# Kernel tuning notes

Hardware: AMD Instinct MI355X
Metric: run time of the kernel (lower is better)

## Reference

```python
import jax, jax.numpy as jnp
import numpy as np


def setup_inputs() -> dict:
    key = jax.random.key(0)
    ks = jax.random.split(key, 5)
    B, DEC, ENC, H = 4, 256, 1024, 256
    s = 1.0 / np.sqrt(H)
    return {
        "x_decoder": jax.random.normal(ks[0], (B, DEC, H), dtype=jnp.float32),
        "x_encoder": jax.random.normal(ks[1], (B, ENC, H), dtype=jnp.float32),
        "w1": jax.random.normal(ks[2], (H, H), dtype=jnp.float32) * s,
        "w2": jax.random.normal(ks[3], (H, H), dtype=jnp.float32) * s,
        "v": jax.random.normal(ks[4], (H,), dtype=jnp.float32) * s,
    }


def reference(x_decoder, x_encoder, w1, w2, v):
    # nn.Linear applies x @ W^T; weights here stored as (out, in) = (H, H)
    enc_t = jnp.einsum('beh,oh->beo', x_encoder, w1)   # (B, ENC, H)
    dec_t = jnp.einsum('bdh,oh->bdo', x_decoder, w2)   # (B, DEC, H)
    # Broadcast-add -> tanh -> dot with v: scores (B, DEC, ENC)
    scores = jnp.einsum('bdeh,h->bde',
                        jnp.tanh(dec_t[:, :, None, :] + enc_t[:, None, :, :]), v)
    return jax.nn.log_softmax(scores, axis=-1)
```

## Files before the change

kernel.cpp:

```cpp
#include <hip/hip_runtime.h>
#include <hip/hip_bf16.h>


#define B_ 4
#define DEC_ 256
#define ENC_ 1024
#define H_ 256

using bf16x8 = __attribute__((ext_vector_type(8))) short;
using f32x4 = __attribute__((ext_vector_type(4))) float;

__device__ inline short f2bf(float f) {
  union { float f; unsigned u; } x; x.f = f;
  return (short)((x.u + 0x8000u) >> 16);
}

#define LDK 72

__global__ __launch_bounds__(256) void gemm_mfma(
    const float* __restrict__ w1, const float* __restrict__ xe,
    const float* __restrict__ xd, const float* __restrict__ w2,
    float* __restrict__ encE, float* __restrict__ decE) {
  const int blk = blockIdx.x;
  const float* A;
  const float* Bsrc;
  float* C;
  int ldc, m0, n0;
  if (blk < 256) {
    const int b = blk >> 6;
    const int t = blk & 63;
    m0 = (t >> 4) << 6; n0 = (t & 15) << 6;
    A = w1;
    Bsrc = xe + (size_t)b * ENC_ * H_;
    C = encE + (size_t)b * H_ * ENC_;
    ldc = ENC_;
  } else {
    const int blk2 = blk - 256;
    const int b = blk2 >> 4;
    const int t = blk2 & 15;
    m0 = (t >> 2) << 6; n0 = (t & 3) << 6;
    A = xd + (size_t)b * DEC_ * H_;
    Bsrc = w2;
    C = decE + (size_t)b * DEC_ * H_;
    ldc = H_;
  }
  const int K = H_;
  const int tid = threadIdx.x;
  const int wave = tid >> 6, lane = tid & 63;
  const int wm = (wave >> 1) << 5, wn = (wave & 1) << 5;
  const int fr = lane & 15;
  const int fk = (lane >> 4) << 3;

  __shared__ short As[2][64][LDK];
  __shared__ short Bs[2][64][LDK];

  const int srow = tid >> 2;
  const int skq = (tid & 3) << 4;
  const float* ag = A + (size_t)(m0 + srow) * K + skq;
  const float* bg = Bsrc + (size_t)(n0 + srow) * K + skq;

  float4 ra[4], rb[4];
#define LDCHUNK(K0)                                                    \
  {                                                                    \
    _Pragma("unroll")                                                  \
    for (int i = 0; i < 4; ++i) {                                      \
      ra[i] = *(const float4*)(ag + (K0) + 4 * i);                     \
      rb[i] = *(const float4*)(bg + (K0) + 4 * i);                     \
    }                                                                  \
  }
#define STCHUNK(BUF)                                                   \
  {                                                                    \
    _Pragma("unroll")                                                  \
    for (int j = 0; j < 2; ++j) {                                      \
      bf16x8 pa, pb;                                                   \
      pa[0] = f2bf(ra[2 * j].x);     pa[1] = f2bf(ra[2 * j].y);        \
      pa[2] = f2bf(ra[2 * j].z);     pa[3] = f2bf(ra[2 * j].w);        \
      pa[4] = f2bf(ra[2 * j + 1].x); pa[5] = f2bf(ra[2 * j + 1].y);    \
      pa[6] = f2bf(ra[2 * j + 1].z); pa[7] = f2bf(ra[2 * j + 1].w);    \
      pb[0] = f2bf(rb[2 * j].x);     pb[1] = f2bf(rb[2 * j].y);        \
      pb[2] = f2bf(rb[2 * j].z);     pb[3] = f2bf(rb[2 * j].w);        \
      pb[4] = f2bf(rb[2 * j + 1].x); pb[5] = f2bf(rb[2 * j + 1].y);    \
      pb[6] = f2bf(rb[2 * j + 1].z); pb[7] = f2bf(rb[2 * j + 1].w);    \
      *(bf16x8*)&As[BUF][srow][skq + 8 * j] = pa;                      \
      *(bf16x8*)&Bs[BUF][srow][skq + 8 * j] = pb;                      \
    }                                                                  \
  }

  f32x4 acc[2][2] = {};

#define COMPUTE(BUF)                                                   \
  {                                                                    \
    _Pragma("unroll")                                                  \
    for (int kk = 0; kk < 2; ++kk) {                                   \
      bf16x8 af[2], bff[2];                                            \
      _Pragma("unroll")                                                \
      for (int mi = 0; mi < 2; ++mi)                                   \
        af[mi] = *(const bf16x8*)&As[BUF][wm + (mi << 4) + fr][(kk << 5) + fk]; \
      _Pragma("unroll")                                                \
      for (int ni = 0; ni < 2; ++ni)                                   \
        bff[ni] = *(const bf16x8*)&Bs[BUF][wn + (ni << 4) + fr][(kk << 5) + fk]; \
      _Pragma("unroll")                                                \
      for (int mi = 0; mi < 2; ++mi)                                   \
        _Pragma("unroll")                                              \
        for (int ni = 0; ni < 2; ++ni)                                 \
          acc[mi][ni] = __builtin_amdgcn_mfma_f32_16x16x32_bf16(       \
              af[mi], bff[ni], acc[mi][ni], 0, 0, 0);                  \
    }                                                                  \
  }

  LDCHUNK(0)
  STCHUNK(0)
  __syncthreads();
  LDCHUNK(64) COMPUTE(0) STCHUNK(1) __syncthreads();
  LDCHUNK(128) COMPUTE(1) STCHUNK(0) __syncthreads();
  LDCHUNK(192) COMPUTE(0) STCHUNK(1) __syncthreads();
  COMPUTE(1)

  const float SC = 2.8853900817779268f;
#pragma unroll
  for (int mi = 0; mi < 2; ++mi) {
#pragma unroll
    for (int ni = 0; ni < 2; ++ni) {
      const int row = m0 + wm + (mi << 4) + ((lane >> 4) << 2);
      const int col = n0 + wn + (ni << 4) + (lane & 15);
#pragma unroll
      for (int r = 0; r < 4; ++r)
        C[(size_t)(row + r) * ldc + col] =
            __builtin_amdgcn_exp2f(acc[mi][ni][r] * SC);
    }
  }
}


#define PROC1(D4, ACC)                                                 \
  {                                                                    \
    const float m0 = fmaf(E0, (D4).x, 1.0f);                           \
    const float m1 = fmaf(E1, (D4).y, 1.0f);                           \
    const float m2 = fmaf(E2, (D4).z, 1.0f);                           \
    const float m3 = fmaf(E3, (D4).w, 1.0f);                           \
    const float pa = m0 * m1, pb = m2 * m3;                            \
    const float n01 = fmaf(wC.x, m1, wC.y * m0);                       \
    const float n23 = fmaf(wC.z, m3, wC.w * m2);                       \
    const float num = fmaf(n01, pb, n23 * pa);                         \
    ACC = fmaf(num, __builtin_amdgcn_rcpf(pa * pb), ACC);              \
  }

__global__ __launch_bounds__(512) void scores_k(
    const float* __restrict__ encE, const float* __restrict__ decE,
    const float* __restrict__ v, float* __restrict__ out) {
  const int bid = blockIdx.x;
  const int xcd = bid & 7;
  const int b = xcd >> 1;
  const int rem = ((bid >> 3) << 1) | (xcd & 1);
  const int es = rem & 15;
  const int d0 = (rem >> 4) << 4;
  const int tid = threadIdx.x;
  const int lane = tid & 63;
  const int wid = __builtin_amdgcn_readfirstlane(tid >> 6);

  const int e = (es << 6) + lane;
  const int d = d0 + (wid << 1);

  const float* ep = encE + (size_t)b * H_ * ENC_ + e;
  const float* dp = decE + (size_t)(b * DEC_ + d) * H_;
  float acc0 = 0.0f, acc1 = 0.0f;

#pragma unroll 8
  for (int g = 0; g < 64; ++g) {
    const int h = g << 2;
    const float E0 = ep[(size_t)h * ENC_];
    const float E1 = ep[(size_t)(h + 1) * ENC_];
    const float E2 = ep[(size_t)(h + 2) * ENC_];
    const float E3 = ep[(size_t)(h + 3) * ENC_];
    const float4 wC = *(const float4*)(v + h);
    const float4 dA = *(const float4*)(dp + h);
    const float4 dB = *(const float4*)(dp + H_ + h);
    PROC1(dA, acc0)
    PROC1(dB, acc1)
  }

  float* orow = out + (size_t)(b * DEC_ + d) * ENC_ + e;
  orow[0] = -2.0f * acc0;
  orow[ENC_] = -2.0f * acc1;
}


__global__ __launch_bounds__(256) void lsm_k(float* __restrict__ out) {
  const int row = blockIdx.x;
  float* p = out + (size_t)row * ENC_;
  const int tid = threadIdx.x;
  const int lane = tid & 63, wid = tid >> 6;

  __shared__ float rm[4], rs[4];

  float4 x = *(const float4*)(p + 4 * tid);

  float m = fmaxf(fmaxf(x.x, x.y), fmaxf(x.z, x.w));
#pragma unroll
  for (int o = 32; o >= 1; o >>= 1) m = fmaxf(m, __shfl_xor(m, o, 64));
  if (lane == 0) rm[wid] = m;
  __syncthreads();
  const float M = fmaxf(fmaxf(rm[0], rm[1]), fmaxf(rm[2], rm[3]));

  const float L2E = 1.4426950408889634f;
  const float LN2 = 0.6931471805599453f;
  float z = __builtin_amdgcn_exp2f((x.x - M) * L2E) +
            __builtin_amdgcn_exp2f((x.y - M) * L2E) +
            __builtin_amdgcn_exp2f((x.z - M) * L2E) +
            __builtin_amdgcn_exp2f((x.w - M) * L2E);
#pragma unroll
  for (int o = 32; o >= 1; o >>= 1) z += __shfl_xor(z, o, 64);
  if (lane == 0) rs[wid] = z;
  __syncthreads();
  const float S = (rs[0] + rs[1]) + (rs[2] + rs[3]);

  const float lse = M + LN2 * __builtin_amdgcn_logf(S);
  x.x -= lse; x.y -= lse; x.z -= lse; x.w -= lse;
  *(float4*)(p + 4 * tid) = x;
}

extern "C" void kernel_launch(void* const* d_in, const int* in_sizes, int n_in,
                              void* d_out, int out_size, void* d_ws, size_t ws_size,
                              hipStream_t stream) {
  const float* xd = (const float*)d_in[0];
  const float* xe = (const float*)d_in[1];
  const float* w1 = (const float*)d_in[2];
  const float* w2 = (const float*)d_in[3];
  const float* v  = (const float*)d_in[4];
  float* out = (float*)d_out;

  float* encE = (float*)d_ws;
  float* decE = encE + (size_t)B_ * H_ * ENC_;

  gemm_mfma<<<320, 256, 0, stream>>>(w1, xe, xd, w2, encE, decE);
  scores_k<<<1024, 512, 0, stream>>>(encE, decE, v, out);
  lsm_k<<<B_ * DEC_, 256, 0, stream>>>(out);
}
```

Measured before the change: 45.39 us.

## Stage encoder tile in LDS and use packed float2 math for scores

Restructures the scores kernel so each block stages a 128-wide encoder slab (transposed, two e-columns per lane) into shared memory in two H halves. Each lane then computes two encoder columns for two decoder rows, using packed float2 arithmetic so the compiler can emit v_pk_fma/v_pk_mul. Decoder and v values become wave-uniform scalar loads, and the grid is halved. The goal is fewer global loads per output and doubled ALU throughput on the rational tanh evaluation. The cost is a 66KB LDS footprint, which limits occupancy, plus extra syncs.

```diff
diff --git a/kernel.cpp b/kernel.cpp
--- a/kernel.cpp
+++ b/kernel.cpp
@@ -9,11 +9,14 @@
 
 using bf16x8 = __attribute__((ext_vector_type(8))) short;
 using f32x4 = __attribute__((ext_vector_type(4))) float;
+using f2 = __attribute__((ext_vector_type(2))) float;
 
 __device__ inline short f2bf(float f) {
   union { float f; unsigned u; } x; x.f = f;
   return (short)((x.u + 0x8000u) >> 16);
 }
+
+__device__ inline f2 bc(float s) { return f2{s, s}; }
 
 #define LDK 72
 
@@ -132,17 +135,21 @@
 }
 
 
-#define PROC1(D4, ACC)                                                 \
-  {                                                                    \
-    const float m0 = fmaf(E0, (D4).x, 1.0f);                           \
-    const float m1 = fmaf(E1, (D4).y, 1.0f);                           \
-    const float m2 = fmaf(E2, (D4).z, 1.0f);                           \
-    const float m3 = fmaf(E3, (D4).w, 1.0f);                           \
-    const float pa = m0 * m1, pb = m2 * m3;                            \
-    const float n01 = fmaf(wC.x, m1, wC.y * m0);                       \
-    const float n23 = fmaf(wC.z, m3, wC.w * m2);                       \
-    const float num = fmaf(n01, pb, n23 * pa);                         \
-    ACC = fmaf(num, __builtin_amdgcn_rcpf(pa * pb), ACC);              \
+#define ESTR 260
+
+#define TANH4(Ea, Eb, Q, W, A0, A1)                                    \
+  {                                                                    \
+    const f2 m0 = f2{Ea.x, Ea.y} * bc(Q[0]) + one;                     \
+    const f2 m1 = f2{Ea.z, Ea.w} * bc(Q[1]) + one;                     \
+    const f2 m2 = f2{Eb.x, Eb.y} * bc(Q[2]) + one;                     \
+    const f2 m3 = f2{Eb.z, Eb.w} * bc(Q[3]) + one;                     \
+    const f2 pa = m0 * m1, pb = m2 * m3;                               \
+    const f2 n01 = bc(W[0]) * m1 + bc(W[1]) * m0;                      \
+    const f2 n23 = bc(W[2]) * m3 + bc(W[3]) * m2;                      \
+    const f2 num = n01 * pb + n23 * pa;                                \
+    const f2 den = pa * pb;                                            \
+    A0 += num.x * __builtin_amdgcn_rcpf(den.x);                        \
+    A1 += num.y * __builtin_amdgcn_rcpf(den.y);                        \
   }
 
 __global__ __launch_bounds__(512) void scores_k(
@@ -152,36 +159,68 @@
   const int xcd = bid & 7;
   const int b = xcd >> 1;
   const int rem = ((bid >> 3) << 1) | (xcd & 1);
-  const int es = rem & 15;
-  const int d0 = (rem >> 4) << 4;
+  const int es = rem & 7;
+  const int dg = rem >> 3;
   const int tid = threadIdx.x;
   const int lane = tid & 63;
-  const int wid = __builtin_amdgcn_readfirstlane(tid >> 6);
-
-  const int e = (es << 6) + lane;
-  const int d = d0 + (wid << 1);
-
-  const float* ep = encE + (size_t)b * H_ * ENC_ + e;
-  const float* dp = decE + (size_t)(b * DEC_ + d) * H_;
-  float acc0 = 0.0f, acc1 = 0.0f;
-
-#pragma unroll 8
-  for (int g = 0; g < 64; ++g) {
-    const int h = g << 2;
-    const float E0 = ep[(size_t)h * ENC_];
-    const float E1 = ep[(size_t)(h + 1) * ENC_];
-    const float E2 = ep[(size_t)(h + 2) * ENC_];
-    const float E3 = ep[(size_t)(h + 3) * ENC_];
-    const float4 wC = *(const float4*)(v + h);
-    const float4 dA = *(const float4*)(dp + h);
-    const float4 dB = *(const float4*)(dp + H_ + h);
-    PROC1(dA, acc0)
-    PROC1(dB, acc1)
-  }
-
-  float* orow = out + (size_t)(b * DEC_ + d) * ENC_ + e;
-  orow[0] = -2.0f * acc0;
-  orow[ENC_] = -2.0f * acc1;
+
+  __shared__ __align__(16) float Es[64 * ESTR];
+
+  const int e0 = es << 7;
+  const int du = __builtin_amdgcn_readfirstlane((dg << 4) + ((tid >> 6) << 1));
+  const float* dp0 = decE + (size_t)(b * DEC_ + du) * H_;
+  const float* dp1 = dp0 + H_;
+
+  float a00 = 0.f, a01 = 0.f, a10 = 0.f, a11 = 0.f;
+  const f2 one = {1.0f, 1.0f};
+
+#define STAGE(C2)                                                      \
+  {                                                                    \
+    const float* src = encE + (size_t)b * H_ * ENC_ +                  \
+                       (size_t)(C2) * 128 * ENC_ + e0;                 \
+    _Pragma("unroll")                                                  \
+    for (int s = 0; s < 8; ++s) {                                      \
+      const int fi = (s << 9) + tid;                      \
+      const int hl = fi >> 5;                              \
+      const int c = fi & 31;                       \
+      const float4 x = *(const float4*)(src + (size_t)hl * ENC_ + (c << 2)); \
+      *(f2*)&Es[(2 * c) * ESTR + 2 * hl] = f2{x.x, x.y};               \
+      *(f2*)&Es[(2 * c + 1) * ESTR + 2 * hl] = f2{x.z, x.w};           \
+    }                                                                  \
+  }
+
+#define CHUNKS(C2)                                                     \
+  {                                                                    \
+    _Pragma("unroll")                                                  \
+    for (int sc = 0; sc < 8; ++sc) {           \
+      const int hb = (C2)*128 + (sc << 4);                             \
+      float q0[16], q1[16], wv[16];                                    \
+      _Pragma("unroll")                                                \
+      for (int i = 0; i < 16; ++i) {                                   \
+        q0[i] = dp0[hb + i]; q1[i] = dp1[hb + i]; wv[i] = v[hb + i];   \
+      }                                                                \
+      _Pragma("unroll")                                                \
+      for (int g = 0; g < 4; ++g) {                    \
+        const int hl = (sc << 4) + (g << 2);        \
+        const float4 Ea = *(const float4*)&Es[lane * ESTR + 2 * hl];   \
+        const float4 Eb = *(const float4*)&Es[lane * ESTR + 2 * hl + 4]; \
+        TANH4(Ea, Eb, (&q0[g << 2]), (&wv[g << 2]), a00, a01)          \
+        TANH4(Ea, Eb, (&q1[g << 2]), (&wv[g << 2]), a10, a11)          \
+      }                                                                \
+    }                                                                  \
+  }
+
+  STAGE(0)
+  __syncthreads();
+  CHUNKS(0)
+  __syncthreads();
+  STAGE(1)
+  __syncthreads();
+  CHUNKS(1)
+
+  float* o0 = out + (size_t)(b * DEC_ + du) * ENC_ + e0 + (lane << 1);
+  *(f2*)o0 = f2{-2.0f * a00, -2.0f * a01};
+  *(f2*)(o0 + ENC_) = f2{-2.0f * a10, -2.0f * a11};
 }
 
 
@@ -233,6 +272,6 @@
   float* decE = encE + (size_t)B_ * H_ * ENC_;
 
   gemm_mfma<<<320, 256, 0, stream>>>(w1, xe, xd, w2, encE, decE);
-  scores_k<<<1024, 512, 0, stream>>>(encE, decE, v, out);
+  scores_k<<<512, 512, 0, stream>>>(encE, decE, v, out);
   lsm_k<<<B_ * DEC_, 256, 0, stream>>>(out);
 }
```

Measured after the change: 45.11 us. About the same (-0.6%).
